# Performance work log

Measured on AMD Instinct MI355X. Metric: run time of the kernel, lower is better.

Reference implementation:

```python
import jax, jax.numpy as jnp
import numpy as np
from jax import lax

B, CIN, COUT, H, W, K = 32, 256, 256, 56, 56, 3

def setup_inputs() -> dict:
    key = jax.random.key(0)
    k1, k2, k3 = jax.random.split(key, 3)
    inp = jax.random.normal(k1, (B, CIN, H, W), dtype=jnp.float32)
    # kaiming-style init for conv kernel, normal init for bias
    fan_in = CIN * K * K
    kernel = jax.random.normal(k2, (COUT, CIN, K, K), dtype=jnp.float32) * np.float32(np.sqrt(2.0 / fan_in))
    bias = jax.random.normal(k3, (COUT,), dtype=jnp.float32)
    return {"inp": inp, "kernel": kernel, "bias": bias}

def reference(inp, kernel, bias):
    # Equivalent to the crossbar path: im2col 3x3 patches @ stacked [kernel|bias]
    # matrix == standard conv2d(padding=1, stride=1) + bias.
    out = lax.conv_general_dilated(
        inp, kernel,
        window_strides=(1, 1),
        padding=((1, 1), (1, 1)),
        dimension_numbers=("NCHW", "OIHW", "NCHW"),
    )
    return out + bias[None, :, None, None]
```

## Files before the change

### kernel.cpp

```cpp
#include <hip/hip_runtime.h>
#include <hip/hip_bf16.h>


#define BB    32
#define CINC  256
#define COUTC 256
#define HH    56
#define WW    56
#define HP    58
#define WP    58
#define PIX_PER_IMG 3136
#define NPIX  100352
#define KTOT  2304
#define NKT   72

#define XT_BYTES ((size_t)BB*HP*WP*CINC*2)
#define WR_ELEMS ((size_t)COUTC*KTOT)
#define WR_BYTES (WR_ELEMS*2)

#define BUF_SZ 24576
#define B_OFF  16384

using frag_t = __attribute__((ext_vector_type(8))) short;
using f32x16 = __attribute__((ext_vector_type(16))) float;

__device__ __forceinline__ void gload_lds16(const void* gsrc, void* ldst) {
  __builtin_amdgcn_global_load_lds(
      (const __attribute__((address_space(1))) unsigned*)gsrc,
      (__attribute__((address_space(3))) unsigned*)ldst, 16, 0, 0);
}

__global__ void xpose_kernel(const float* __restrict__ inp,
                             __hip_bfloat16* __restrict__ xt) {
  int bid = blockIdx.x;
  int hp = bid % HP;
  int t  = bid / HP;
  int cb = t % 4;
  int b  = t / 4;
  __shared__ __hip_bfloat16 tile[64 * 60];
  int tid = threadIdx.x;
  for (int i = tid; i < 64 * 60; i += 256) tile[i] = __float2bfloat16(0.f);
  __syncthreads();
  int h = hp - 1;
  if (h >= 0 && h < HH) {
    const float* src = inp + ((size_t)(b * CINC + cb * 64) * HH + h) * WW;
    for (int i = tid; i < 64 * WW; i += 256) {
      int ci = i / WW, w = i - ci * WW;
      tile[ci * 60 + (w + 1)] = __float2bfloat16(src[(size_t)ci * HH * WW + w]);
    }
  }
  __syncthreads();
  __hip_bfloat16* dst = xt + ((size_t)(b * HP + hp) * WP) * CINC + cb * 64;
  for (int i = tid; i < WP * 64; i += 256) {
    int wp = i >> 6, ci = i & 63;
    dst[(size_t)wp * CINC + ci] = tile[ci * 60 + wp];
  }
}

__global__ void wprep_kernel(const float* __restrict__ k4,
                             __hip_bfloat16* __restrict__ wr) {
  int i = blockIdx.x * 256 + threadIdx.x;
  if (i >= (int)WR_ELEMS) return;
  int co = i / KTOT;
  int k  = i - co * KTOT;
  int tap = k >> 8;
  int ci  = k & 255;
  wr[i] = __float2bfloat16(k4[(co * CINC + ci) * 9 + tap]);
}

__global__ __launch_bounds__(256, 2) void conv_mfma32(
    const __hip_bfloat16* __restrict__ xt,
    const __hip_bfloat16* __restrict__ wr,
    const float* __restrict__ bias,
    float* __restrict__ out) {
  __shared__ alignas(16) char lds[3 * BUF_SZ];

  const int tid  = threadIdx.x;
  const int lane = tid & 63;
  const int wid  = tid >> 6;
  const int wm   = wid >> 1;
  const int wn   = wid & 1;
  const int l31  = lane & 31;
  const int lhi  = lane >> 5;

  const int bid   = blockIdx.x;
  const int ntile = (bid & 7) * 98 + (bid >> 3);

  const char* wr_b = (const char*)wr;
  const char* xt_b = (const char*)xt;

  const int lr = lane >> 2;
  const int sc = (((lane & 3) ^ (lr & 3)) << 4);

  const char* pA0 = wr_b + (size_t)(wid * 64 +  0 + lr) * (KTOT * 2) + sc;
  const char* pA1 = wr_b + (size_t)(wid * 64 + 16 + lr) * (KTOT * 2) + sc;
  const char* pA2 = wr_b + (size_t)(wid * 64 + 32 + lr) * (KTOT * 2) + sc;
  const char* pA3 = wr_b + (size_t)(wid * 64 + 48 + lr) * (KTOT * 2) + sc;

  auto mkB = [&](int jb) -> const char* {
    int px = ntile * 128 + (wid * 2 + jb) * 16 + lr;
    int b  = px / PIX_PER_IMG;
    int hw = px - b * PIX_PER_IMG;
    int h = hw / WW, w = hw - h * WW;
    return xt_b + (size_t)((b * HP + h) * WP + w) * (CINC * 2) + sc;
  };
  const char* pB0 = mkB(0);
  const char* pB1 = mkB(1);

#define STG_A(WB, T2) {                                                    \
    size_t _ao = (size_t)(T2) * 64;                                        \
    gload_lds16(pA0 + _ao, lds + (WB)*BUF_SZ + (wid * 4 + 0) * 1024);      \
    gload_lds16(pA1 + _ao, lds + (WB)*BUF_SZ + (wid * 4 + 1) * 1024);      \
    gload_lds16(pA2 + _ao, lds + (WB)*BUF_SZ + (wid * 4 + 2) * 1024); }

#define STG_B(WB, T2) {                                                    \
    int _tap = (T2) >> 3; int _rr = _tap / 3, _ss = _tap - _rr * 3;        \
    size_t _ao = (size_t)(T2) * 64;                                        \
    size_t _bo = (size_t)(_rr * WP + _ss) * (CINC * 2)                     \
               + (size_t)((T2) & 7) * 64;                                  \
    gload_lds16(pA3 + _ao, lds + (WB)*BUF_SZ + (wid * 4 + 3) * 1024);      \
    gload_lds16(pB0 + _bo, lds + (WB)*BUF_SZ + B_OFF + (wid*2+0) * 1024);  \
    gload_lds16(pB1 + _bo, lds + (WB)*BUF_SZ + B_OFF + (wid*2+1) * 1024); }

  const int aoff  = (wm * 128 + l31) * 64;
  const int boffr = (wn * 64 + l31) * 64;
  const int ck0   = ((lhi ^ (l31 & 3)) << 4);
  const int ck1   = (((2 + lhi) ^ (l31 & 3)) << 4);

  frag_t fa0[4], fb0[2], fa1[4], fb1[2];
  f32x16 acc[4][2] = {};

#define RSL(RB, CK, FA, FB) {                                              \
    const char* _b = lds + (RB)*BUF_SZ;                                    \
    _Pragma("unroll") for (int m = 0; m < 4; ++m)                          \
      FA[m] = *(const frag_t*)(_b + aoff + m * 2048 + (CK));               \
    _Pragma("unroll") for (int n = 0; n < 2; ++n)                          \
      FB[n] = *(const frag_t*)(_b + B_OFF + boffr + n * 2048 + (CK)); }

#define MF(FA, FB) {                                                       \
    _Pragma("unroll") for (int m = 0; m < 4; ++m)                          \
    _Pragma("unroll") for (int n = 0; n < 2; ++n)                          \
      acc[m][n] = __builtin_amdgcn_mfma_f32_32x32x16_bf16(                 \
          FA[m], FB[n], acc[m][n], 0, 0, 0); }

#define BODY(T, RB, WB, NB) {                                              \
    RSL(RB, ck1, fa1, fb1);                                                \
    STG_A(WB, (T) + 2);                                                    \
    MF(fa0, fb0);                                                          \
    STG_B(WB, (T) + 2);                                                    \
    asm volatile("s_waitcnt lgkmcnt(0)" ::: "memory");                     \
    asm volatile("s_waitcnt vmcnt(6)" ::: "memory");                       \
    __builtin_amdgcn_s_barrier();                                          \
    __builtin_amdgcn_sched_barrier(0);                                     \
    RSL(NB, ck0, fa0, fb0);                                                \
    MF(fa1, fb1); }

  STG_A(0, 0); STG_B(0, 0);
  STG_A(1, 1); STG_B(1, 1);
  asm volatile("s_waitcnt vmcnt(6)" ::: "memory");
  __builtin_amdgcn_s_barrier();
  __builtin_amdgcn_sched_barrier(0);
  RSL(0, ck0, fa0, fb0);

  for (int base = 0; base < 69; base += 3) {
    BODY(base + 0, 0, 2, 1);
    BODY(base + 1, 1, 0, 2);
    BODY(base + 2, 2, 1, 0);
  }
  BODY(69, 0, 2, 1);

  {
    RSL(1, ck1, fa1, fb1);
    MF(fa0, fb0);
    asm volatile("s_waitcnt lgkmcnt(0)" ::: "memory");
    asm volatile("s_waitcnt vmcnt(0)" ::: "memory");
    __builtin_amdgcn_s_barrier();
    __builtin_amdgcn_sched_barrier(0);
    RSL(2, ck0, fa0, fb0);
    MF(fa1, fb1);
  }
  {
    RSL(2, ck1, fa1, fb1);
    MF(fa0, fb0);
    MF(fa1, fb1);
  }

  int pb[2], phw[2];
#pragma unroll
  for (int n = 0; n < 2; ++n) {
    int pxg = ntile * 128 + wn * 64 + n * 32 + l31;
    pb[n]  = pxg / PIX_PER_IMG;
    phw[n] = pxg - pb[n] * PIX_PER_IMG;
  }
#pragma unroll
  for (int m = 0; m < 4; ++m) {
#pragma unroll
    for (int r = 0; r < 16; ++r) {
      int co = wm * 128 + m * 32 + (r & 3) + 8 * (r >> 2) + 4 * lhi;
      float bv = bias[co];
#pragma unroll
      for (int n = 0; n < 2; ++n)
        out[((size_t)pb[n] * COUTC + co) * PIX_PER_IMG + phw[n]] =
            acc[m][n][r] + bv;
    }
  }
}

__global__ void conv_direct(const float* __restrict__ inp,
                            const float* __restrict__ kern,
                            const float* __restrict__ bias,
                            float* __restrict__ out) {
  int idx = blockIdx.x * 256 + threadIdx.x;
  if (idx >= BB * COUTC * PIX_PER_IMG) return;
  int w = idx % WW;
  int t = idx / WW;
  int h = t % HH; t /= HH;
  int co = t % COUTC;
  int b  = t / COUTC;
  float acc = bias[co];
  for (int ci = 0; ci < CINC; ++ci)
    for (int r = 0; r < 3; ++r) {
      int hh = h + r - 1;
      if (hh < 0 || hh >= HH) continue;
      for (int s = 0; s < 3; ++s) {
        int ww2 = w + s - 1;
        if (ww2 < 0 || ww2 >= WW) continue;
        acc += inp[((size_t)(b * CINC + ci) * HH + hh) * WW + ww2] *
               kern[(co * CINC + ci) * 9 + r * 3 + s];
      }
    }
  out[idx] = acc;
}

extern "C" void kernel_launch(void* const* d_in, const int* in_sizes, int n_in,
                              void* d_out, int out_size, void* d_ws, size_t ws_size,
                              hipStream_t stream) {
  const float* inp  = (const float*)d_in[0];
  const float* kern = (const float*)d_in[1];
  const float* bias = (const float*)d_in[2];
  float* out = (float*)d_out;

  size_t need = XT_BYTES + WR_BYTES;
  if (ws_size < need) {
    int tot = BB * COUTC * PIX_PER_IMG;
    conv_direct<<<(tot + 255) / 256, 256, 0, stream>>>(inp, kern, bias, out);
    return;
  }

  __hip_bfloat16* xt  = (__hip_bfloat16*)d_ws;
  __hip_bfloat16* wrp = (__hip_bfloat16*)((char*)d_ws + XT_BYTES);

  xpose_kernel<<<BB * 4 * HP, 256, 0, stream>>>(inp, xt);
  wprep_kernel<<<(int)((WR_ELEMS + 255) / 256), 256, 0, stream>>>(kern, wrp);
  conv_mfma32<<<NPIX / 128, 256, 0, stream>>>(xt, wrp, bias, out);
}
```

Measured before the change: 196.6 us.

## Switch conv GEMM to 16x16x32 MFMA with single-stage fragment pipeline

Replaces the 32x32x16 bf16 MFMA tiling with 16x16x32 MFMA. Each wave now holds an 8x4 grid of 4-wide accumulators and reads the full 32-wide K slice in one LDS pass per stage. The LDS swizzle changes to a rotation pattern to match the new fragment read layout. The register double-buffered fragment prefetch across barriers is dropped, and s_setprio is raised around the MFMA burst. The aim is better MFMA issue efficiency and less LDS bank conflict, at the cost of losing the overlap between LDS reads and MFMA across stages.

Result: faster. 186.0 us (-5.4%).

```diff
diff --git a/kernel.cpp b/kernel.cpp
--- a/kernel.cpp
+++ b/kernel.cpp
@@ -22,7 +22,7 @@
 #define B_OFF  16384
 
 using frag_t = __attribute__((ext_vector_type(8))) short;
-using f32x16 = __attribute__((ext_vector_type(16))) float;
+using f32x4  = __attribute__((ext_vector_type(4))) float;
 
 __device__ __forceinline__ void gload_lds16(const void* gsrc, void* ldst) {
   __builtin_amdgcn_global_load_lds(
@@ -68,7 +68,7 @@
   wr[i] = __float2bfloat16(k4[(co * CINC + ci) * 9 + tap]);
 }
 
-__global__ __launch_bounds__(256, 2) void conv_mfma32(
+__global__ __launch_bounds__(256, 2) void conv_p16(
     const __hip_bfloat16* __restrict__ xt,
     const __hip_bfloat16* __restrict__ wr,
     const float* __restrict__ bias,
@@ -80,8 +80,8 @@
   const int wid  = tid >> 6;
   const int wm   = wid >> 1;
   const int wn   = wid & 1;
-  const int l31  = lane & 31;
-  const int lhi  = lane >> 5;
+  const int fr   = lane & 15;
+  const int g    = lane >> 4;
 
   const int bid   = blockIdx.x;
   const int ntile = (bid & 7) * 98 + (bid >> 3);
@@ -89,8 +89,8 @@
   const char* wr_b = (const char*)wr;
   const char* xt_b = (const char*)xt;
 
-  const int lr = lane >> 2;
-  const int sc = (((lane & 3) ^ (lr & 3)) << 4);
+  const int lr  = lane >> 2;
+  const int sc  = ((((lane & 3) - ((lane >> 3) & 3)) & 3) << 4);
 
   const char* pA0 = wr_b + (size_t)(wid * 64 +  0 + lr) * (KTOT * 2) + sc;
   const char* pA1 = wr_b + (size_t)(wid * 64 + 16 + lr) * (KTOT * 2) + sc;
@@ -98,7 +98,7 @@
   const char* pA3 = wr_b + (size_t)(wid * 64 + 48 + lr) * (KTOT * 2) + sc;
 
   auto mkB = [&](int jb) -> const char* {
-    int px = ntile * 128 + (wid * 2 + jb) * 16 + lr;
+    int px = ntile * 128 + wid * 32 + jb * 16 + lr;
     int b  = px / PIX_PER_IMG;
     int hw = px - b * PIX_PER_IMG;
     int h = hw / WW, w = hw - h * WW;
@@ -107,101 +107,90 @@
   const char* pB0 = mkB(0);
   const char* pB1 = mkB(1);
 
-#define STG_A(WB, T2) {                                                    \
+#define STG(T2, WB) {                                                      \
     size_t _ao = (size_t)(T2) * 64;                                        \
-    gload_lds16(pA0 + _ao, lds + (WB)*BUF_SZ + (wid * 4 + 0) * 1024);      \
-    gload_lds16(pA1 + _ao, lds + (WB)*BUF_SZ + (wid * 4 + 1) * 1024);      \
-    gload_lds16(pA2 + _ao, lds + (WB)*BUF_SZ + (wid * 4 + 2) * 1024); }
-
-#define STG_B(WB, T2) {                                                    \
     int _tap = (T2) >> 3; int _rr = _tap / 3, _ss = _tap - _rr * 3;        \
-    size_t _ao = (size_t)(T2) * 64;                                        \
     size_t _bo = (size_t)(_rr * WP + _ss) * (CINC * 2)                     \
                + (size_t)((T2) & 7) * 64;                                  \
-    gload_lds16(pA3 + _ao, lds + (WB)*BUF_SZ + (wid * 4 + 3) * 1024);      \
-    gload_lds16(pB0 + _bo, lds + (WB)*BUF_SZ + B_OFF + (wid*2+0) * 1024);  \
-    gload_lds16(pB1 + _bo, lds + (WB)*BUF_SZ + B_OFF + (wid*2+1) * 1024); }
-
-  const int aoff  = (wm * 128 + l31) * 64;
-  const int boffr = (wn * 64 + l31) * 64;
-  const int ck0   = ((lhi ^ (l31 & 3)) << 4);
-  const int ck1   = (((2 + lhi) ^ (l31 & 3)) << 4);
-
-  frag_t fa0[4], fb0[2], fa1[4], fb1[2];
-  f32x16 acc[4][2] = {};
-
-#define RSL(RB, CK, FA, FB) {                                              \
-    const char* _b = lds + (RB)*BUF_SZ;                                    \
-    _Pragma("unroll") for (int m = 0; m < 4; ++m)                          \
-      FA[m] = *(const frag_t*)(_b + aoff + m * 2048 + (CK));               \
-    _Pragma("unroll") for (int n = 0; n < 2; ++n)                          \
-      FB[n] = *(const frag_t*)(_b + B_OFF + boffr + n * 2048 + (CK)); }
-
-#define MF(FA, FB) {                                                       \
-    _Pragma("unroll") for (int m = 0; m < 4; ++m)                          \
-    _Pragma("unroll") for (int n = 0; n < 2; ++n)                          \
-      acc[m][n] = __builtin_amdgcn_mfma_f32_32x32x16_bf16(                 \
-          FA[m], FB[n], acc[m][n], 0, 0, 0); }
-
-#define BODY(T, RB, WB, NB) {                                              \
-    RSL(RB, ck1, fa1, fb1);                                                \
-    STG_A(WB, (T) + 2);                                                    \
-    MF(fa0, fb0);                                                          \
-    STG_B(WB, (T) + 2);                                                    \
-    asm volatile("s_waitcnt lgkmcnt(0)" ::: "memory");                     \
+    char* _d = lds + (WB) * BUF_SZ;                                        \
+    gload_lds16(pA0 + _ao, _d + wid * 4096 + 0);                           \
+    gload_lds16(pA1 + _ao, _d + wid * 4096 + 1024);                        \
+    gload_lds16(pA2 + _ao, _d + wid * 4096 + 2048);                        \
+    gload_lds16(pA3 + _ao, _d + wid * 4096 + 3072);                        \
+    gload_lds16(pB0 + _bo, _d + B_OFF + wid * 2048 + 0);                   \
+    gload_lds16(pB1 + _bo, _d + B_OFF + wid * 2048 + 1024); }
+
+  const int ckr   = (((g + (fr >> 1)) & 3) << 4);
+  const int aroff = (wm * 128 + fr) * 64 + ckr;
+  const int broff = B_OFF + (wn * 64 + fr) * 64 + ckr;
+
+  frag_t fa[8], fb[4];
+  f32x4 acc[8][4] = {};
+
+#define RSL(RB) {                                                          \
+    const char* _b = lds + (RB) * BUF_SZ;                                  \
+    _Pragma("unroll") for (int m = 0; m < 8; ++m)                          \
+      fa[m] = *(const frag_t*)(_b + aroff + m * 1024);                     \
+    _Pragma("unroll") for (int n = 0; n < 4; ++n)                          \
+      fb[n] = *(const frag_t*)(_b + broff + n * 1024); }
+
+#define MF() {                                                             \
+    __builtin_amdgcn_s_setprio(1);                                         \
+    _Pragma("unroll") for (int m = 0; m < 8; ++m)                          \
+    _Pragma("unroll") for (int n = 0; n < 4; ++n)                          \
+      acc[m][n] = __builtin_amdgcn_mfma_f32_16x16x32_bf16(                 \
+          fa[m], fb[n], acc[m][n], 0, 0, 0);                               \
+    __builtin_amdgcn_s_setprio(0); }
+
+#define BODY(T, RB, WB) {                                                  \
+    STG((T) + 2, WB);                                                      \
+    RSL(RB);                                                               \
+    MF();                                                                  \
     asm volatile("s_waitcnt vmcnt(6)" ::: "memory");                       \
     __builtin_amdgcn_s_barrier();                                          \
-    __builtin_amdgcn_sched_barrier(0);                                     \
-    RSL(NB, ck0, fa0, fb0);                                                \
-    MF(fa1, fb1); }
-
-  STG_A(0, 0); STG_B(0, 0);
-  STG_A(1, 1); STG_B(1, 1);
+    __builtin_amdgcn_sched_barrier(0); }
+
+  STG(0, 0);
+  STG(1, 1);
   asm volatile("s_waitcnt vmcnt(6)" ::: "memory");
   __builtin_amdgcn_s_barrier();
   __builtin_amdgcn_sched_barrier(0);
-  RSL(0, ck0, fa0, fb0);
 
   for (int base = 0; base < 69; base += 3) {
-    BODY(base + 0, 0, 2, 1);
-    BODY(base + 1, 1, 0, 2);
-    BODY(base + 2, 2, 1, 0);
-  }
-  BODY(69, 0, 2, 1);
-
+    BODY(base + 0, 0, 2);
+    BODY(base + 1, 1, 0);
+    BODY(base + 2, 2, 1);
+  }
+  BODY(69, 0, 2);
   {
-    RSL(1, ck1, fa1, fb1);
-    MF(fa0, fb0);
-    asm volatile("s_waitcnt lgkmcnt(0)" ::: "memory");
+    RSL(1);
+    MF();
     asm volatile("s_waitcnt vmcnt(0)" ::: "memory");
     __builtin_amdgcn_s_barrier();
     __builtin_amdgcn_sched_barrier(0);
-    RSL(2, ck0, fa0, fb0);
-    MF(fa1, fb1);
   }
   {
-    RSL(2, ck1, fa1, fb1);
-    MF(fa0, fb0);
-    MF(fa1, fb1);
-  }
-
-  int pb[2], phw[2];
-#pragma unroll
-  for (int n = 0; n < 2; ++n) {
-    int pxg = ntile * 128 + wn * 64 + n * 32 + l31;
+    RSL(2);
+    MF();
+  }
+
+  int pb[4], phw[4];
+#pragma unroll
+  for (int n = 0; n < 4; ++n) {
+    int pxg = ntile * 128 + wn * 64 + n * 16 + fr;
     pb[n]  = pxg / PIX_PER_IMG;
     phw[n] = pxg - pb[n] * PIX_PER_IMG;
   }
 #pragma unroll
-  for (int m = 0; m < 4; ++m) {
-#pragma unroll
-    for (int r = 0; r < 16; ++r) {
-      int co = wm * 128 + m * 32 + (r & 3) + 8 * (r >> 2) + 4 * lhi;
+  for (int m = 0; m < 8; ++m) {
+#pragma unroll
+    for (int rg = 0; rg < 4; ++rg) {
+      int co = wm * 128 + m * 16 + g * 4 + rg;
       float bv = bias[co];
 #pragma unroll
-      for (int n = 0; n < 2; ++n)
+      for (int n = 0; n < 4; ++n)
         out[((size_t)pb[n] * COUTC + co) * PIX_PER_IMG + phw[n]] =
-            acc[m][n][r] + bv;
+            acc[m][n][rg] + bv;
     }
   }
 }
@@ -252,5 +241,5 @@
 
   xpose_kernel<<<BB * 4 * HP, 256, 0, stream>>>(inp, xt);
   wprep_kernel<<<(int)((WR_ELEMS + 255) / 256), 256, 0, stream>>>(kern, wrp);
-  conv_mfma32<<<NPIX / 128, 256, 0, stream>>>(xt, wrp, bias, out);
-}
+  conv_p16<<<NPIX / 128, 256, 0, stream>>>(xt, wrp, bias, out);
+}
```
